# Kernel tuning notes

Hardware: AMD Instinct MI355X
Metric: run time of the kernel (lower is better)

The kernel has to match this reference:

```python
import jax, jax.numpy as jnp
import numpy as np

N_NODES = 20000
N_EDGES = 240000
N_GRAPHS = 200
D_IN = 118
H = 256          # simplified hidden width standing in for the mul=50 irreps hidden
NB = 10          # number_of_basis
RH = 100         # fc_neurons hidden
L = 3            # layers
SH = 9           # lmax=2 -> 1+3+5 spherical-harmonic channels
MAX_RADIUS = 5.0
NUM_NEIGHBORS = 12.0


def setup_inputs() -> dict:
    key = jax.random.key(0)
    ks = jax.random.split(key, 16)
    inp = {
        "x": jax.random.normal(ks[0], (N_NODES, D_IN), jnp.float32),
        "pos": jax.random.normal(ks[1], (N_NODES, 3), jnp.float32),
        "edge_shift": jax.random.normal(ks[2], (N_EDGES, 3), jnp.float32),
        "lattice": jax.random.normal(ks[3], (N_GRAPHS, 3, 3), jnp.float32),
        "W_embed": jax.random.normal(ks[4], (D_IN, H), jnp.float32) / np.sqrt(D_IN),
        "r1": jax.random.normal(ks[5], (L, NB, RH), jnp.float32) / np.sqrt(NB),
        "b1": jax.random.normal(ks[6], (L, RH), jnp.float32) * 0.1,
        "r2": jax.random.normal(ks[7], (L, RH, H), jnp.float32) / np.sqrt(RH),
        "Wtp": jax.random.normal(ks[8], (L, SH, H, H), jnp.float32) / np.sqrt(SH * H),
        "Wself": jax.random.normal(ks[9], (L, H, H), jnp.float32) / np.sqrt(H),
        "Wskip": jax.random.normal(ks[10], (L, H, H), jnp.float32) / np.sqrt(H),
        "Wout": jax.random.normal(ks[11], (H, 1), jnp.float32) / np.sqrt(H),
        "edge_index": jax.random.randint(ks[12], (2, N_EDGES), 0, N_NODES, jnp.int64)
                        if jax.config.jax_enable_x64 else
                      jax.random.randint(ks[12], (2, N_EDGES), 0, N_NODES).astype(jnp.int32),
        "batch": jnp.sort(jax.random.randint(ks[13], (N_NODES,), 0, N_GRAPHS)).astype(jnp.int32),
    }
    return inp


def _sph_harm_lmax2(u):
    """Component-normalized real spherical harmonics up to l=2 on unit vectors u [E,3]."""
    x, y, z = u[:, 0], u[:, 1], u[:, 2]
    c1 = np.sqrt(3.0)
    c2 = np.sqrt(15.0)
    return jnp.stack([
        jnp.ones_like(x),                       # l=0
        c1 * x, c1 * y, c1 * z,                 # l=1
        c2 * x * y, c2 * y * z,                 # l=2
        (np.sqrt(5.0) / 2.0) * (3.0 * z * z - 1.0),
        c2 * x * z, (c2 / 2.0) * (x * x - y * y),
    ], axis=1)                                  # [E, 9]


def _soft_one_hot_cosine(lens):
    """e3nn soft_one_hot_linspace(basis='cosine', cutoff=True) * sqrt(NB)."""
    vals = jnp.linspace(0.0, MAX_RADIUS, NB + 2)
    step = vals[1] - vals[0]
    vals = vals[1:-1]
    diff = (lens[:, None] - vals[None, :]) / step          # [E, NB]
    emb = jnp.cos(0.5 * jnp.pi * diff) * (diff > -1.0) * (diff < 1.0)
    return emb * np.sqrt(float(NB))


def _forward(x, pos, edge_shift, lattice, W_embed, r1, b1, r2, Wtp, Wself, Wskip, Wout,
             edge_src, edge_dst, batch):
    edge_batch = batch[edge_src]                            # [E]
    # periodic edge vectors: pos[dst] - pos[src] + shift @ lattice[graph]
    edge_vec = pos[edge_dst] - pos[edge_src] + jnp.einsum(
        'ni,nij->nj', edge_shift, lattice[edge_batch])      # [E, 3]
    lens = jnp.linalg.norm(edge_vec, axis=1)                # [E]
    u = edge_vec / (lens[:, None] + 1e-12)
    sh = _sph_harm_lmax2(u)                                 # [E, 9]
    emb = _soft_one_hot_cosine(lens)                        # [E, NB]

    h = x @ W_embed                                         # [N, H]
    inv_sqrt_deg = 1.0 / np.sqrt(NUM_NEIGHBORS)
    for l in range(L):
        radial = jax.nn.silu(emb @ r1[l] + b1[l]) @ r2[l]   # [E, H]
        hs = h[edge_src] * radial                           # gather + radial gate
        # weighted tensor-product-like message: sum_a (hs * sh_a) @ Wtp[l, a]
        msg = (hs * sh[:, 0:1]) @ Wtp[l, 0]
        for a in range(1, SH):
            msg = msg + (hs * sh[:, a:a + 1]) @ Wtp[l, a]   # [E, H]
        agg = jax.ops.segment_sum(msg, edge_dst, num_segments=N_NODES) * inv_sqrt_deg
        h = jax.nn.gelu(agg @ Wself[l] + h @ Wskip[l])      # [N, H]

    node_out = h @ Wout                                     # [N, 1]
    # scatter_mean over graphs
    sums = jax.ops.segment_sum(node_out, batch, num_segments=N_GRAPHS)
    cnts = jax.ops.segment_sum(jnp.ones((N_NODES, 1), node_out.dtype), batch,
                               num_segments=N_GRAPHS)
    return sums / jnp.maximum(cnts, 1.0)                    # [G, 1]


def reference(x, pos, edge_shift, lattice, W_embed, r1, b1, r2, Wtp, Wself, Wskip, Wout,
              edge_index, batch):
    return _forward(x, pos, edge_shift, lattice, W_embed, r1, b1, r2, Wtp, Wself, Wskip,
                    Wout, edge_index[0], edge_index[1], batch)
```

## Files before the change

kernel.cpp:

```cpp
#include <hip/hip_runtime.h>
#include <hip/hip_bf16.h>
#include <cstddef>
#include <cstdint>

#define NNODE  20000
#define MPAD   20096
#define NEDGE  240000
#define NGRAPH 200
#define DIN    118
#define HD     256
#define NBASIS 10
#define RHID   100
#define NLAYER 3
#define NSH    9
#define SHSTR  16
#define KTP    (NSH * HD)
#define KTOT   (KTP + HD)
#define KR2    128
#define KEMB   128
#define NRT    (MPAD / 64)

typedef _Float16 f16;
typedef _Float16 f16x2 __attribute__((ext_vector_type(2)));
typedef _Float16 f16x4 __attribute__((ext_vector_type(4)));
typedef _Float16 f16x8 __attribute__((ext_vector_type(8)));
typedef float    f32x4 __attribute__((ext_vector_type(4)));

__device__ __forceinline__ float gelu_tanh(float v) {
  float v3 = v * v * v;
  return 0.5f * v * (1.f + tanhf(0.7978845608028654f * (v + 0.044715f * v3)));
}

__device__ __forceinline__ void gload16(const void* g, void* l) {
  __builtin_amdgcn_global_load_lds(
      (const __attribute__((address_space(1))) unsigned int*)g,
      (__attribute__((address_space(3))) unsigned int*)l, 16, 0, 0);
}

__device__ __forceinline__ int perm64(int rho) {
  return (rho & ~63) | ((rho & 15) * 4 + ((rho >> 4) & 3));
}
__device__ __forceinline__ int inv_perm64(int n) {
  return (n & ~63) | (((n & 3) << 4) | ((n >> 2) & 15));
}

__global__ void deg_hist_kernel(const int* __restrict__ ei, int* __restrict__ deg)
{
  int e = blockIdx.x * 256 + threadIdx.x;
  if (e >= NEDGE) return;
  atomicAdd(&deg[ei[NEDGE + e]], 1);
}

__global__ void scan_kernel(const int* __restrict__ deg, int* __restrict__ rowptr)
{
  __shared__ int part[256];
  int t = threadIdx.x;
  const int chunk = (NNODE + 255) / 256;
  int start = t * chunk;
  int end = min(start + chunk, NNODE);
  int s = 0;
  for (int i = start; i < end; ++i) s += deg[i];
  part[t] = s;
  __syncthreads();
  for (int off = 1; off < 256; off <<= 1) {
    int v = (t >= off) ? part[t - off] : 0;
    __syncthreads();
    part[t] += v;
    __syncthreads();
  }
  int run = (t == 0) ? 0 : part[t - 1];
  for (int i = start; i < end; ++i) { rowptr[i] = run; run += deg[i]; }
  if (t == 255) rowptr[NNODE] = run;
}

__global__ void edge_geom_kernel(const float* __restrict__ pos,
                                 const float* __restrict__ shift,
                                 const float* __restrict__ lat,
                                 const int* __restrict__ ei,
                                 const int* __restrict__ batch,
                                 const int* __restrict__ rowptr,
                                 int* __restrict__ cursor,
                                 f16* __restrict__ sh_s,
                                 float* __restrict__ lens_s)
{
  int e = blockIdx.x * 256 + threadIdx.x;
  if (e >= NEDGE) return;
  int src = ei[e];
  int dst = ei[NEDGE + e];
  int b = batch[src];
  const float* L = lat + (size_t)b * 9;
  float s0 = shift[e * 3 + 0], s1 = shift[e * 3 + 1], s2 = shift[e * 3 + 2];
  float ev[3];
#pragma unroll
  for (int j = 0; j < 3; ++j)
    ev[j] = pos[dst * 3 + j] - pos[src * 3 + j] + s0 * L[j] + s1 * L[3 + j] + s2 * L[6 + j];
  float len = sqrtf(ev[0] * ev[0] + ev[1] * ev[1] + ev[2] * ev[2]);
  float inv = 1.f / (len + 1e-12f);
  float x = ev[0] * inv, y = ev[1] * inv, z = ev[2] * inv;
  const float c1 = 1.7320508075688772f;
  const float c2 = 3.872983346207417f;
  int p = atomicAdd(&cursor[dst], 1);
  int si = rowptr[dst] + p;
  f16* she = sh_s + (size_t)si * SHSTR;
  she[0] = (f16)1.f;
  she[1] = (f16)(c1 * x);
  she[2] = (f16)(c1 * y);
  she[3] = (f16)(c1 * z);
  she[4] = (f16)(c2 * x * y);
  she[5] = (f16)(c2 * y * z);
  she[6] = (f16)(1.1180339887498949f * (3.f * z * z - 1.f));
  she[7] = (f16)(c2 * x * z);
  she[8] = (f16)(1.9364916731037085f * (x * x - y * y));
  she[9] = (f16)0.f;
  *(int*)(she + 10) = src;
  she[12] = (f16)0.f; she[13] = (f16)0.f; she[14] = (f16)0.f; she[15] = (f16)0.f;
  lens_s[si] = len;
}

__global__ void prep_kernel(const float* __restrict__ Wtp_l,
                            const float* __restrict__ Wself_l,
                            const float* __restrict__ Wskip_l,
                            const float* __restrict__ r2l,
                            const float* __restrict__ r1l,
                            const float* __restrict__ b1l,
                            f16* __restrict__ Wtp16,
                            f16* __restrict__ WselfT16,
                            f16* __restrict__ Bcat,
                            f16* __restrict__ r2h,
                            f16* __restrict__ r1h)
{
  int b = blockIdx.x, t = threadIdx.x;
  if (b < KTP) {
    int i = b * 256 + t;
    Wtp16[i] = (f16)Wtp_l[i];
  } else if (b < KTP + 256) {
    int n = b - KTP;
    WselfT16[(size_t)n * HD + t] = (f16)(Wself_l[(size_t)t * HD + n] * 0.28867513459481287f);
  } else if (b < KTP + 512) {
    int rho = b - KTP - 256;
    int pcol = perm64(rho);
    Bcat[(size_t)rho * KTOT + KTP + t] = (f16)Wskip_l[(size_t)t * HD + pcol];
  } else if (b < KTP + 768) {
    int rho = b - KTP - 512;
    if (t < KR2) {
      int p = perm64(rho);
      r2h[(size_t)rho * KR2 + t] = (t < RHID) ? (f16)r2l[(size_t)t * HD + p] : (f16)0.f;
    }
  } else {
#pragma unroll
    for (int u = 0; u < 16; ++u) {
      int idx = u * 256 + t;
      int n = idx >> 5, j = idx & 31;
      float v = 0.f;
      if (n < RHID) {
        if (j < NBASIS) v = r1l[(size_t)j * RHID + n];
        else if (j == NBASIS) v = b1l[n];
      }
      r1h[idx] = (f16)v;
    }
  }
}

__global__ void convert_x_kernel(const float* __restrict__ x, f16* __restrict__ xh)
{
  int i = blockIdx.x * 2 + (threadIdx.x >> 7);
  int k = threadIdx.x & 127;
  xh[(size_t)i * KEMB + k] = (i < NNODE && k < DIN) ? (f16)x[(size_t)i * DIN + k] : (f16)0.f;
}

__global__ void convert_wemb_kernel(const float* __restrict__ Wemb, f16* __restrict__ WembT16)
{
  int n = blockIdx.x, k = threadIdx.x;
  WembT16[(size_t)n * KEMB + k] = (k < DIN) ? (f16)Wemb[(size_t)k * HD + n] : (f16)0.f;
}

__global__ __launch_bounds__(256) void gemm_nt_kernel(
    const f16* __restrict__ A, const f16* __restrict__ B,
    f16* __restrict__ C, int K, int ldc, int permRows)
{
  __shared__ __align__(16) f16 As[4][64][8];
  __shared__ __align__(16) f16 Bs[4][128][8];
  int t = threadIdx.x;
  int lane = t & 63, w = t >> 6;
  int row0 = blockIdx.x * 64;
  int n0 = blockIdx.y * 128;
  f32x4 acc[2][4];
#pragma unroll
  for (int i = 0; i < 2; ++i)
#pragma unroll
    for (int j = 0; j < 4; ++j) acc[i][j] = (f32x4){0.f, 0.f, 0.f, 0.f};
  int mq = (w & 1) * 32, nq = (w >> 1) * 64;
  for (int k0 = 0; k0 < K; k0 += 32) {
    {
      int row = t & 63, cc = t >> 6;
      *(uint4*)&As[cc][row][0] = *(const uint4*)(A + (size_t)(row0 + row) * K + k0 + cc * 8);
    }
#pragma unroll
    for (int u = 0; u < 2; ++u) {
      int idx = t + u * 256;
      int ch = idx >> 7, nn = idx & 127;
      *(uint4*)&Bs[ch][nn][0] = *(const uint4*)(B + (size_t)(n0 + nn) * K + k0 + ch * 8);
    }
    __syncthreads();
    int q = lane >> 4, r = lane & 15;
    f16x8 af[2], bfr[4];
#pragma unroll
    for (int i = 0; i < 2; ++i) af[i] = *(const f16x8*)&As[q][mq + i * 16 + r][0];
#pragma unroll
    for (int j = 0; j < 4; ++j) bfr[j] = *(const f16x8*)&Bs[q][nq + j * 16 + r][0];
#pragma unroll
    for (int i = 0; i < 2; ++i)
#pragma unroll
      for (int j = 0; j < 4; ++j)
        acc[i][j] = __builtin_amdgcn_mfma_f32_16x16x32_f16(af[i], bfr[j], acc[i][j], 0, 0, 0);
    __syncthreads();
  }
  int q4 = ((lane >> 4)) * 4, cl = lane & 15;
#pragma unroll
  for (int i = 0; i < 2; ++i)
#pragma unroll
    for (int rr = 0; rr < 4; ++rr) {
      int row = row0 + mq + i * 16 + q4 + rr;
      int orow = permRows ? inv_perm64(row) : row;
#pragma unroll
      for (int j = 0; j < 4; ++j)
        C[(size_t)orow * ldc + n0 + nq + j * 16 + cl] = (f16)acc[i][j][rr];
    }
}

#define RHSTR 136
__global__ __launch_bounds__(256) void radial_kernel(
    const float* __restrict__ lens_s,
    const f16* __restrict__ sh_s,
    const f16* __restrict__ h,
    const f16* __restrict__ r1h,
    const f16* __restrict__ r2h,
    f16* __restrict__ hs)
{
  __shared__ __align__(16) f16 emb_s[64][40];
  __shared__ __align__(16) f16 rhA[64 * RHSTR];
  __shared__ int srcs[64];
  int t = threadIdx.x;
  int lane = t & 63, w = t >> 6;
  int r = lane & 15, q = lane >> 4;
  int e0 = blockIdx.x * 64;

  if (t < 64) srcs[t] = *(const int*)(sh_s + (size_t)(e0 + t) * SHSTR + 10);

  {
    float len = lens_s[e0 + lane];
    const float step = 5.f / 11.f;
    const float sq = 3.1622776601683795f;
    f16x8 v;
#pragma unroll
    for (int kk = 0; kk < 8; ++kk) {
      int j = w * 8 + kk;
      float val = 0.f;
      if (j < NBASIS) {
        float d = (len - (float)(j + 1) * step) / step;
        val = (d > -1.f && d < 1.f) ? (__cosf(1.5707963267948966f * d) * sq) : 0.f;
      } else if (j == NBASIS) {
        val = 1.f;
      }
      v[kk] = (f16)val;
    }
    *(f16x8*)&emb_s[lane][w * 8] = v;
  }

  int n0w = w * 64;
  f16x8 bfr[4][4];
#pragma unroll
  for (int j = 0; j < 4; ++j)
#pragma unroll
    for (int ks = 0; ks < 4; ++ks)
      bfr[j][ks] = *(const f16x8*)(r2h + (size_t)(n0w + j * 16 + r) * KR2 + ks * 32 + q * 8);

  f16x8 b1f[2];
#pragma unroll
  for (int j = 0; j < 2; ++j)
    b1f[j] = *(const f16x8*)(r1h + (size_t)((2 * w + j) * 16 + r) * 32 + q * 8);

  __syncthreads();

  f32x4 acc1[4][2];
#pragma unroll
  for (int i = 0; i < 4; ++i)
#pragma unroll
    for (int j = 0; j < 2; ++j) acc1[i][j] = (f32x4){0.f, 0.f, 0.f, 0.f};
  {
    f16x8 a1f[4];
#pragma unroll
    for (int i = 0; i < 4; ++i)
      a1f[i] = *(const f16x8*)&emb_s[i * 16 + r][q * 8];
#pragma unroll
    for (int i = 0; i < 4; ++i)
#pragma unroll
      for (int j = 0; j < 2; ++j)
        acc1[i][j] = __builtin_amdgcn_mfma_f32_16x16x32_f16(a1f[i], b1f[j], acc1[i][j], 0, 0, 0);
  }

#pragma unroll
  for (int i = 0; i < 4; ++i)
#pragma unroll
    for (int j = 0; j < 2; ++j)
#pragma unroll
      for (int rr = 0; rr < 4; ++rr) {
        float s = acc1[i][j][rr];
        s = __fdividef(s, 1.f + __expf(-s));
        rhA[(i * 16 + q * 4 + rr) * RHSTR + (2 * w + j) * 16 + r] = (f16)s;
      }
  __syncthreads();

  f16x4 hv[4][4];
#pragma unroll
  for (int i = 0; i < 4; ++i)
#pragma unroll
    for (int rr = 0; rr < 4; ++rr) {
      int m = i * 16 + q * 4 + rr;
      hv[i][rr] = *(const f16x4*)(h + (size_t)srcs[m] * HD + n0w + r * 4);
    }

  f32x4 acc[4][4];
#pragma unroll
  for (int i = 0; i < 4; ++i)
#pragma unroll
    for (int j = 0; j < 4; ++j) acc[i][j] = (f32x4){0.f, 0.f, 0.f, 0.f};
#pragma unroll
  for (int ks = 0; ks < 4; ++ks) {
    f16x8 af[4];
#pragma unroll
    for (int i = 0; i < 4; ++i)
      af[i] = *(const f16x8*)&rhA[(i * 16 + r) * RHSTR + ks * 32 + q * 8];
#pragma unroll
    for (int i = 0; i < 4; ++i)
#pragma unroll
      for (int j = 0; j < 4; ++j)
        acc[i][j] = __builtin_amdgcn_mfma_f32_16x16x32_f16(af[i], bfr[j][ks], acc[i][j], 0, 0, 0);
  }

#pragma unroll
  for (int i = 0; i < 4; ++i)
#pragma unroll
    for (int rr = 0; rr < 4; ++rr) {
      int m = i * 16 + q * 4 + rr;
      f16x4 o;
#pragma unroll
      for (int j = 0; j < 4; ++j)
        o[j] = (f16)(acc[i][j][rr] * (float)hv[i][rr][j]);
      *(f16x4*)(hs + (size_t)(e0 + m) * HD + n0w + r * 4) = o;
    }
}

__global__ __launch_bounds__(256) void gather2_kernel(
    const int* __restrict__ rowptr, const f16* __restrict__ hs,
    const f16* __restrict__ sh_s,
    f16* __restrict__ T)
{
  int t = threadIdx.x;
  int half = t >> 7, lc = t & 127;
  int base = blockIdx.x * 4;
  for (int s = 0; s < 2; ++s) {
    int n = base + s * 2 + half;
    int beg = rowptr[n], end = rowptr[n + 1];
    float a0[NSH], a1[NSH];
#pragma unroll
    for (int a = 0; a < NSH; ++a) { a0[a] = 0.f; a1[a] = 0.f; }
    int j = beg;
    for (; j + 2 <= end; j += 2) {
      const f16* she0 = sh_s + (size_t)j * SHSTR;
      const f16* she1 = she0 + SHSTR;
      f16x8 s80 = *(const f16x8*)she0;
      f16x8 s81 = *(const f16x8*)she1;
      float s8v0 = (float)she0[8];
      float s8v1 = (float)she1[8];
      f16x2 rv0 = *(const f16x2*)(hs + (size_t)j * HD + 2 * lc);
      f16x2 rv1 = *(const f16x2*)(hs + (size_t)(j + 1) * HD + 2 * lc);
      float p00 = (float)rv0[0];
      float p01 = (float)rv0[1];
      float p10 = (float)rv1[0];
      float p11 = (float)rv1[1];
#pragma unroll
      for (int a = 0; a < 8; ++a) {
        float sv0 = (float)s80[a], sv1 = (float)s81[a];
        a0[a] += sv0 * p00 + sv1 * p10;
        a1[a] += sv0 * p01 + sv1 * p11;
      }
      a0[8] += s8v0 * p00 + s8v1 * p10;
      a1[8] += s8v0 * p01 + s8v1 * p11;
    }
    if (j < end) {
      const f16* she = sh_s + (size_t)j * SHSTR;
      f16x8 s8 = *(const f16x8*)she;
      float s8v = (float)she[8];
      f16x2 rv = *(const f16x2*)(hs + (size_t)j * HD + 2 * lc);
      float p0 = (float)rv[0];
      float p1 = (float)rv[1];
#pragma unroll
      for (int a = 0; a < 8; ++a) {
        float sv = (float)s8[a];
        a0[a] += sv * p0; a1[a] += sv * p1;
      }
      a0[8] += s8v * p0; a1[8] += s8v * p1;
    }
    f16* Tn = T + (size_t)n * KTP + 2 * lc;
#pragma unroll
    for (int a = 0; a < NSH; ++a) {
      f16x2 o; o[0] = (f16)a0[a]; o[1] = (f16)a1[a];
      *(f16x2*)(Tn + a * HD) = o;
    }
  }
}

#define GBM 64
#define GBN 128
#define BK  64
#define NKSTEP (KTOT / BK)
__global__ __launch_bounds__(256) void gemm_fused_kernel(
    const f16* __restrict__ A1,
    const f16* __restrict__ A2,
    const f16* __restrict__ B,
    f16* __restrict__ C)
{
  __shared__ __align__(16) f16 As[2][GBM][8][8];
  __shared__ __align__(16) f16 Bs[2][GBN][8][8];
  int t = threadIdx.x;
  int lane = t & 63, w = t >> 6;
  int row0 = blockIdx.x * GBM;
  int n0 = blockIdx.y * GBN;
  int mq = (w & 1) * 32, nq = (w >> 1) * 64;
  int q = lane >> 4, r = lane & 15;

  f32x4 acc[2][4];
#pragma unroll
  for (int i = 0; i < 2; ++i)
#pragma unroll
    for (int j = 0; j < 4; ++j) acc[i][j] = (f32x4){0.f, 0.f, 0.f, 0.f};

  auto stage = [&](int buf, int k0) {
#pragma unroll
    for (int u = 0; u < 2; ++u) {
      int idx = u * 256 + t;
      int row = idx >> 3, chg = (idx & 7) ^ (row & 7);
      const f16* ga = (k0 < KTP)
          ? (A1 + (size_t)(row0 + row) * KTP + k0 + chg * 8)
          : (A2 + (size_t)(row0 + row) * HD + (k0 - KTP) + chg * 8);
      gload16(ga, &As[buf][0][0][0] + (size_t)(u * 256 + w * 64) * 8);
    }
#pragma unroll
    for (int u = 0; u < 4; ++u) {
      int idx = u * 256 + t;
      int row = idx >> 3, chg = (idx & 7) ^ (row & 7);
      const f16* gb = B + (size_t)(n0 + row) * KTOT + k0 + chg * 8;
      gload16(gb, &Bs[buf][0][0][0] + (size_t)(u * 256 + w * 64) * 8);
    }
  };

  stage(0, 0);
  __syncthreads();

  int cur = 0;
  for (int s = 0; s < NKSTEP; ++s) {
    if (s + 1 < NKSTEP) stage(cur ^ 1, (s + 1) * BK);
#pragma unroll
    for (int kk = 0; kk < 2; ++kk) {
      f16x8 af[2], bfr[4];
#pragma unroll
      for (int i = 0; i < 2; ++i) {
        int row = mq + i * 16 + r;
        af[i] = *(const f16x8*)&As[cur][row][(kk * 4 + q) ^ (row & 7)][0];
      }
#pragma unroll
      for (int j = 0; j < 4; ++j) {
        int row = nq + j * 16 + r;
        bfr[j] = *(const f16x8*)&Bs[cur][row][(kk * 4 + q) ^ (row & 7)][0];
      }
#pragma unroll
      for (int i = 0; i < 2; ++i)
#pragma unroll
        for (int j = 0; j < 4; ++j)
          acc[i][j] = __builtin_amdgcn_mfma_f32_16x16x32_f16(af[i], bfr[j], acc[i][j], 0, 0, 0);
    }
    __syncthreads();
    cur ^= 1;
  }

  int q4 = (lane >> 4) * 4, cl = lane & 15;
#pragma unroll
  for (int i = 0; i < 2; ++i)
#pragma unroll
    for (int rr = 0; rr < 4; ++rr) {
      int row = row0 + mq + i * 16 + q4 + rr;
      f16x4 o;
#pragma unroll
      for (int j = 0; j < 4; ++j) o[j] = (f16)gelu_tanh(acc[i][j][rr]);
      *(f16x4*)(C + (size_t)row * HD + n0 + nq + cl * 4) = o;
    }
}

__global__ __launch_bounds__(256) void node_out_fused_kernel(
    const f16* __restrict__ h,
    const float* __restrict__ Wout,
    const int* __restrict__ batch,
    float* __restrict__ out)
{
  __shared__ float red[256];
  int g = blockIdx.x;
  int t = threadIdx.x;
  int lo = 0, hi = NNODE;
  while (lo < hi) { int mid = (lo + hi) >> 1; if (batch[mid] < g) lo = mid + 1; else hi = mid; }
  int start = lo;
  hi = NNODE;
  while (lo < hi) { int mid = (lo + hi) >> 1; if (batch[mid] < g + 1) lo = mid + 1; else hi = mid; }
  int end = lo;
  int half = t >> 7, lc = t & 127;
  float a0 = 0.f, a1 = 0.f;
  for (int n = start + half; n < end; n += 2) {
    f16x2 v = *(const f16x2*)(h + (size_t)n * HD + 2 * lc);
    a0 += (float)v[0];
    a1 += (float)v[1];
  }
  red[t] = a0 * Wout[2 * lc] + a1 * Wout[2 * lc + 1];
  for (int off = 128; off > 0; off >>= 1) {
    __syncthreads();
    if (t < off) red[t] += red[t + off];
  }
  if (t == 0) out[g] = red[0] / fmaxf((float)(end - start), 1.f);
}

extern "C" void kernel_launch(void* const* d_in, const int* in_sizes, int n_in,
                              void* d_out, int out_size, void* d_ws, size_t ws_size,
                              hipStream_t stream)
{
  (void)in_sizes; (void)n_in; (void)out_size;
  const float* x     = (const float*)d_in[0];
  const float* pos   = (const float*)d_in[1];
  const float* shift = (const float*)d_in[2];
  const float* lat   = (const float*)d_in[3];
  const float* Wemb  = (const float*)d_in[4];
  const float* r1    = (const float*)d_in[5];
  const float* b1    = (const float*)d_in[6];
  const float* r2    = (const float*)d_in[7];
  const float* Wtp   = (const float*)d_in[8];
  const float* Wself = (const float*)d_in[9];
  const float* Wskip = (const float*)d_in[10];
  const float* Wout  = (const float*)d_in[11];
  const int*   eidx  = (const int*)d_in[12];
  const int*   batch = (const int*)d_in[13];
  float* out = (float*)d_out;

  char* ws = (char*)d_ws;
  size_t off = 0;
  auto alloc = [&](size_t bytes) -> char* {
    char* p = ws + off;
    off += (bytes + 255) & ~(size_t)255;
    return p;
  };
  f16*   sh_s    = (f16*)alloc((size_t)NEDGE * SHSTR * 2);
  float* lens_s  = (float*)alloc((size_t)NEDGE * 4);
  f16*   hA      = (f16*)alloc((size_t)MPAD * HD * 2);
  f16*   hB      = (f16*)alloc((size_t)MPAD * HD * 2);
  f16*   T       = (f16*)alloc((size_t)MPAD * KTP * 2);
  f16*   rad     = (f16*)alloc((size_t)NEDGE * HD * 2);
  f16*   Bcat    = (f16*)alloc((size_t)HD * KTOT * 2);
  f16*   r2h     = (f16*)alloc((size_t)HD * KR2 * 2);
  f16*   r1hb    = (f16*)alloc((size_t)128 * 32 * 2);
  f16*   Wtp16   = (f16*)alloc((size_t)KTP * HD * 2);
  f16*   WselfT16= (f16*)alloc((size_t)HD * HD * 2);
  int*   rowptr  = (int*)alloc((size_t)(NNODE + 1) * 4);
  int*   deg     = (int*)alloc((size_t)NNODE * 4);
  int*   cursor  = (int*)alloc((size_t)NNODE * 4);
  if (off > ws_size) return;

  f16*   xh      = rad;
  f16*   WembT16 = rad + (size_t)MPAD * KEMB;

  hipMemsetAsync(deg, 0, (size_t)NNODE * 4, stream);
  hipMemsetAsync(cursor, 0, (size_t)NNODE * 4, stream);

  const int EB = (NEDGE + 255) / 256;
  deg_hist_kernel<<<EB, 256, 0, stream>>>(eidx, deg);
  scan_kernel<<<1, 256, 0, stream>>>(deg, rowptr);
  edge_geom_kernel<<<EB, 256, 0, stream>>>(pos, shift, lat, eidx, batch,
                                           rowptr, cursor, sh_s, lens_s);

  convert_x_kernel<<<MPAD / 2, 256, 0, stream>>>(x, xh);
  convert_wemb_kernel<<<HD, KEMB, 0, stream>>>(Wemb, WembT16);
  {
    dim3 eg(MPAD / 64, HD / 128);
    gemm_nt_kernel<<<eg, 256, 0, stream>>>(xh, WembT16, hA, KEMB, HD, 0);
  }

  f16* hcur = hA;
  f16* hnxt = hB;
  dim3 fgrid(NRT, 2);
  dim3 wgrid(HD / 64, KTP / 128);
  for (int l = 0; l < NLAYER; ++l) {
    const float* r1l = r1 + (size_t)l * NBASIS * RHID;
    const float* b1l = b1 + (size_t)l * RHID;
    const float* r2l = r2 + (size_t)l * RHID * HD;
    const float* Wtp_l = Wtp + (size_t)l * NSH * HD * HD;
    const float* Wself_l = Wself + (size_t)l * HD * HD;
    const float* Wskip_l = Wskip + (size_t)l * HD * HD;

    prep_kernel<<<KTP + 768 + 1, 256, 0, stream>>>(Wtp_l, Wself_l, Wskip_l, r2l,
                                                   r1l, b1l,
                                                   Wtp16, WselfT16, Bcat, r2h, r1hb);
    gemm_nt_kernel<<<wgrid, 256, 0, stream>>>(WselfT16, Wtp16, Bcat, HD, KTOT, 1);

    radial_kernel<<<NEDGE / 64, 256, 0, stream>>>(lens_s, sh_s, hcur, r1hb, r2h, rad);
    gather2_kernel<<<NNODE / 4, 256, 0, stream>>>(rowptr, rad, sh_s, T);
    gemm_fused_kernel<<<fgrid, 256, 0, stream>>>(T, hcur, Bcat, hnxt);
    f16* tmp = hcur; hcur = hnxt; hnxt = tmp;
  }

  node_out_fused_kernel<<<NGRAPH, 256, 0, stream>>>(hcur, Wout, batch, out);
}
```

Before: 668.9 us.

## Make radial kernel grid-stride persistent and shrink fused GEMM M-tile to 32

The radial kernel now runs a grid-stride loop over 64-edge tiles with a fixed grid of 1875 blocks. Each block loads its r1/r2 weight fragments into registers once and reuses them across two edge tiles, at the cost of an extra barrier per tile. The fused GEMM M-tile drops from 64 to 32 rows, with each wave owning a 32x32 output piece and the epilogue column mapping adjusted to match. This doubles the number of blocks for better CU occupancy and load balance, but each block fetches the same B tile for half as many rows, so B traffic doubles.

```diff
diff --git a/kernel.cpp b/kernel.cpp
--- a/kernel.cpp
+++ b/kernel.cpp
@@ -243,112 +243,112 @@
   int t = threadIdx.x;
   int lane = t & 63, w = t >> 6;
   int r = lane & 15, q = lane >> 4;
-  int e0 = blockIdx.x * 64;
-
-  if (t < 64) srcs[t] = *(const int*)(sh_s + (size_t)(e0 + t) * SHSTR + 10);
-
-  {
-    float len = lens_s[e0 + lane];
-    const float step = 5.f / 11.f;
-    const float sq = 3.1622776601683795f;
-    f16x8 v;
-#pragma unroll
-    for (int kk = 0; kk < 8; ++kk) {
-      int j = w * 8 + kk;
-      float val = 0.f;
-      if (j < NBASIS) {
-        float d = (len - (float)(j + 1) * step) / step;
-        val = (d > -1.f && d < 1.f) ? (__cosf(1.5707963267948966f * d) * sq) : 0.f;
-      } else if (j == NBASIS) {
-        val = 1.f;
-      }
-      v[kk] = (f16)val;
-    }
-    *(f16x8*)&emb_s[lane][w * 8] = v;
-  }
-
   int n0w = w * 64;
+
   f16x8 bfr[4][4];
 #pragma unroll
   for (int j = 0; j < 4; ++j)
 #pragma unroll
     for (int ks = 0; ks < 4; ++ks)
       bfr[j][ks] = *(const f16x8*)(r2h + (size_t)(n0w + j * 16 + r) * KR2 + ks * 32 + q * 8);
-
   f16x8 b1f[2];
 #pragma unroll
   for (int j = 0; j < 2; ++j)
     b1f[j] = *(const f16x8*)(r1h + (size_t)((2 * w + j) * 16 + r) * 32 + q * 8);
 
-  __syncthreads();
-
-  f32x4 acc1[4][2];
-#pragma unroll
-  for (int i = 0; i < 4; ++i)
-#pragma unroll
-    for (int j = 0; j < 2; ++j) acc1[i][j] = (f32x4){0.f, 0.f, 0.f, 0.f};
-  {
-    f16x8 a1f[4];
+  for (int e0 = blockIdx.x * 64; e0 < NEDGE; e0 += gridDim.x * 64) {
+    if (t < 64) srcs[t] = *(const int*)(sh_s + (size_t)(e0 + t) * SHSTR + 10);
+
+    {
+      float len = lens_s[e0 + lane];
+      const float step = 5.f / 11.f;
+      const float sq = 3.1622776601683795f;
+      f16x8 v;
+#pragma unroll
+      for (int kk = 0; kk < 8; ++kk) {
+        int j = w * 8 + kk;
+        float val = 0.f;
+        if (j < NBASIS) {
+          float d = (len - (float)(j + 1) * step) / step;
+          val = (d > -1.f && d < 1.f) ? (__cosf(1.5707963267948966f * d) * sq) : 0.f;
+        } else if (j == NBASIS) {
+          val = 1.f;
+        }
+        v[kk] = (f16)val;
+      }
+      *(f16x8*)&emb_s[lane][w * 8] = v;
+    }
+    __syncthreads();
+
+    f32x4 acc1[4][2];
 #pragma unroll
     for (int i = 0; i < 4; ++i)
-      a1f[i] = *(const f16x8*)&emb_s[i * 16 + r][q * 8];
+#pragma unroll
+      for (int j = 0; j < 2; ++j) acc1[i][j] = (f32x4){0.f, 0.f, 0.f, 0.f};
+    {
+      f16x8 a1f[4];
+#pragma unroll
+      for (int i = 0; i < 4; ++i)
+        a1f[i] = *(const f16x8*)&emb_s[i * 16 + r][q * 8];
+#pragma unroll
+      for (int i = 0; i < 4; ++i)
+#pragma unroll
+        for (int j = 0; j < 2; ++j)
+          acc1[i][j] = __builtin_amdgcn_mfma_f32_16x16x32_f16(a1f[i], b1f[j], acc1[i][j], 0, 0, 0);
+    }
+
 #pragma unroll
     for (int i = 0; i < 4; ++i)
 #pragma unroll
       for (int j = 0; j < 2; ++j)
-        acc1[i][j] = __builtin_amdgcn_mfma_f32_16x16x32_f16(a1f[i], b1f[j], acc1[i][j], 0, 0, 0);
-  }
-
-#pragma unroll
-  for (int i = 0; i < 4; ++i)
-#pragma unroll
-    for (int j = 0; j < 2; ++j)
+#pragma unroll
+        for (int rr = 0; rr < 4; ++rr) {
+          float s = acc1[i][j][rr];
+          s = __fdividef(s, 1.f + __expf(-s));
+          rhA[(i * 16 + q * 4 + rr) * RHSTR + (2 * w + j) * 16 + r] = (f16)s;
+        }
+    __syncthreads();
+
+    f16x4 hv[4][4];
+#pragma unroll
+    for (int i = 0; i < 4; ++i)
 #pragma unroll
       for (int rr = 0; rr < 4; ++rr) {
-        float s = acc1[i][j][rr];
-        s = __fdividef(s, 1.f + __expf(-s));
-        rhA[(i * 16 + q * 4 + rr) * RHSTR + (2 * w + j) * 16 + r] = (f16)s;
-      }
-  __syncthreads();
-
-  f16x4 hv[4][4];
-#pragma unroll
-  for (int i = 0; i < 4; ++i)
-#pragma unroll
-    for (int rr = 0; rr < 4; ++rr) {
-      int m = i * 16 + q * 4 + rr;
-      hv[i][rr] = *(const f16x4*)(h + (size_t)srcs[m] * HD + n0w + r * 4);
-    }
-
-  f32x4 acc[4][4];
-#pragma unroll
-  for (int i = 0; i < 4; ++i)
-#pragma unroll
-    for (int j = 0; j < 4; ++j) acc[i][j] = (f32x4){0.f, 0.f, 0.f, 0.f};
-#pragma unroll
-  for (int ks = 0; ks < 4; ++ks) {
-    f16x8 af[4];
+        int m = i * 16 + q * 4 + rr;
+        hv[i][rr] = *(const f16x4*)(h + (size_t)srcs[m] * HD + n0w + r * 4);
+      }
+
+    f32x4 acc[4][4];
 #pragma unroll
     for (int i = 0; i < 4; ++i)
-      af[i] = *(const f16x8*)&rhA[(i * 16 + r) * RHSTR + ks * 32 + q * 8];
+#pragma unroll
+      for (int j = 0; j < 4; ++j) acc[i][j] = (f32x4){0.f, 0.f, 0.f, 0.f};
+#pragma unroll
+    for (int ks = 0; ks < 4; ++ks) {
+      f16x8 af[4];
+#pragma unroll
+      for (int i = 0; i < 4; ++i)
+        af[i] = *(const f16x8*)&rhA[(i * 16 + r) * RHSTR + ks * 32 + q * 8];
+#pragma unroll
+      for (int i = 0; i < 4; ++i)
+#pragma unroll
+        for (int j = 0; j < 4; ++j)
+          acc[i][j] = __builtin_amdgcn_mfma_f32_16x16x32_f16(af[i], bfr[j][ks], acc[i][j], 0, 0, 0);
+    }
+
 #pragma unroll
     for (int i = 0; i < 4; ++i)
 #pragma unroll
-      for (int j = 0; j < 4; ++j)
-        acc[i][j] = __builtin_amdgcn_mfma_f32_16x16x32_f16(af[i], bfr[j][ks], acc[i][j], 0, 0, 0);
-  }
-
-#pragma unroll
-  for (int i = 0; i < 4; ++i)
-#pragma unroll
-    for (int rr = 0; rr < 4; ++rr) {
-      int m = i * 16 + q * 4 + rr;
-      f16x4 o;
-#pragma unroll
-      for (int j = 0; j < 4; ++j)
-        o[j] = (f16)(acc[i][j][rr] * (float)hv[i][rr][j]);
-      *(f16x4*)(hs + (size_t)(e0 + m) * HD + n0w + r * 4) = o;
-    }
+      for (int rr = 0; rr < 4; ++rr) {
+        int m = i * 16 + q * 4 + rr;
+        f16x4 o;
+#pragma unroll
+        for (int j = 0; j < 4; ++j)
+          o[j] = (f16)(acc[i][j][rr] * (float)hv[i][rr][j]);
+        *(f16x4*)(hs + (size_t)(e0 + m) * HD + n0w + r * 4) = o;
+      }
+    __syncthreads();
+  }
 }
 
 __global__ __launch_bounds__(256) void gather2_kernel(
@@ -411,7 +411,7 @@
   }
 }
 
-#define GBM 64
+#define GBM 32
 #define GBN 128
 #define BK  64
 #define NKSTEP (KTOT / BK)
@@ -427,24 +427,22 @@
   int lane = t & 63, w = t >> 6;
   int row0 = blockIdx.x * GBM;
   int n0 = blockIdx.y * GBN;
-  int mq = (w & 1) * 32, nq = (w >> 1) * 64;
   int q = lane >> 4, r = lane & 15;
-
-  f32x4 acc[2][4];
+  int nq = w * 32;
+
+  f32x4 acc[2][2];
 #pragma unroll
   for (int i = 0; i < 2; ++i)
 #pragma unroll
-    for (int j = 0; j < 4; ++j) acc[i][j] = (f32x4){0.f, 0.f, 0.f, 0.f};
+    for (int j = 0; j < 2; ++j) acc[i][j] = (f32x4){0.f, 0.f, 0.f, 0.f};
 
   auto stage = [&](int buf, int k0) {
-#pragma unroll
-    for (int u = 0; u < 2; ++u) {
-      int idx = u * 256 + t;
-      int row = idx >> 3, chg = (idx & 7) ^ (row & 7);
+    {
+      int row = t >> 3, chg = (t & 7) ^ (row & 7);
       const f16* ga = (k0 < KTP)
           ? (A1 + (size_t)(row0 + row) * KTP + k0 + chg * 8)
           : (A2 + (size_t)(row0 + row) * HD + (k0 - KTP) + chg * 8);
-      gload16(ga, &As[buf][0][0][0] + (size_t)(u * 256 + w * 64) * 8);
+      gload16(ga, &As[buf][0][0][0] + (size_t)(w * 64) * 8);
     }
 #pragma unroll
     for (int u = 0; u < 4; ++u) {
@@ -463,37 +461,38 @@
     if (s + 1 < NKSTEP) stage(cur ^ 1, (s + 1) * BK);
 #pragma unroll
     for (int kk = 0; kk < 2; ++kk) {
-      f16x8 af[2], bfr[4];
+      f16x8 af[2], bf[2];
 #pragma unroll
       for (int i = 0; i < 2; ++i) {
-        int row = mq + i * 16 + r;
+        int row = i * 16 + r;
         af[i] = *(const f16x8*)&As[cur][row][(kk * 4 + q) ^ (row & 7)][0];
       }
 #pragma unroll
-      for (int j = 0; j < 4; ++j) {
+      for (int j = 0; j < 2; ++j) {
         int row = nq + j * 16 + r;
-        bfr[j] = *(const f16x8*)&Bs[cur][row][(kk * 4 + q) ^ (row & 7)][0];
+        bf[j] = *(const f16x8*)&Bs[cur][row][(kk * 4 + q) ^ (row & 7)][0];
       }
 #pragma unroll
       for (int i = 0; i < 2; ++i)
 #pragma unroll
-        for (int j = 0; j < 4; ++j)
-          acc[i][j] = __builtin_amdgcn_mfma_f32_16x16x32_f16(af[i], bfr[j], acc[i][j], 0, 0, 0);
+        for (int j = 0; j < 2; ++j)
+          acc[i][j] = __builtin_amdgcn_mfma_f32_16x16x32_f16(af[i], bf[j], acc[i][j], 0, 0, 0);
     }
     __syncthreads();
     cur ^= 1;
   }
 
-  int q4 = (lane >> 4) * 4, cl = lane & 15;
+  int q4 = q * 4, cl = r;
+  int colbase = n0 + (w >> 1) * 64 + (w & 1) * 2;
 #pragma unroll
   for (int i = 0; i < 2; ++i)
 #pragma unroll
     for (int rr = 0; rr < 4; ++rr) {
-      int row = row0 + mq + i * 16 + q4 + rr;
-      f16x4 o;
-#pragma unroll
-      for (int j = 0; j < 4; ++j) o[j] = (f16)gelu_tanh(acc[i][j][rr]);
-      *(f16x4*)(C + (size_t)row * HD + n0 + nq + cl * 4) = o;
+      int row = row0 + i * 16 + q4 + rr;
+      f16x2 o;
+      o[0] = (f16)gelu_tanh(acc[i][0][rr]);
+      o[1] = (f16)gelu_tanh(acc[i][1][rr]);
+      *(f16x2*)(C + (size_t)row * HD + colbase + cl * 4) = o;
     }
 }
 
@@ -592,7 +591,7 @@
 
   f16* hcur = hA;
   f16* hnxt = hB;
-  dim3 fgrid(NRT, 2);
+  dim3 fgrid(MPAD / GBM, 2);
   dim3 wgrid(HD / 64, KTP / 128);
   for (int l = 0; l < NLAYER; ++l) {
     const float* r1l = r1 + (size_t)l * NBASIS * RHID;
@@ -607,7 +606,7 @@
                                                    Wtp16, WselfT16, Bcat, r2h, r1hb);
     gemm_nt_kernel<<<wgrid, 256, 0, stream>>>(WselfT16, Wtp16, Bcat, HD, KTOT, 1);
 
-    radial_kernel<<<NEDGE / 64, 256, 0, stream>>>(lens_s, sh_s, hcur, r1hb, r2h, rad);
+    radial_kernel<<<1875, 256, 0, stream>>>(lens_s, sh_s, hcur, r1hb, r2h, rad);
     gather2_kernel<<<NNODE / 4, 256, 0, stream>>>(rowptr, rad, sh_s, T);
     gemm_fused_kernel<<<fgrid, 256, 0, stream>>>(T, hcur, Bcat, hnxt);
     f16* tmp = hcur; hcur = hnxt; hnxt = tmp;
```

New measurement: 758.6 us. 1.13x slower.
